# Kernel tuning notes

Hardware: AMD Instinct MI355X
Metric: run time of the kernel (lower is better)

The kernel has to match this reference:

```python
import jax, jax.numpy as jnp
import numpy as np

B, N, C_IN = 16, 1024, 768
H, KQ, VD = 8, 256, 512          # num_heads, kq_dim, v_dim per head
NH_V = H * VD                    # 4096
D_OUT = 512
SCALE = D_OUT ** -0.5            # module uses dim_out**-0.5
EPS = 1e-5


def _bn(x, gamma, beta, mean, var):
    # eval-mode BatchNorm1d over last dim
    return (x - mean) * (gamma * jax.lax.rsqrt(var + EPS)) + beta


def setup_inputs() -> dict:
    key = jax.random.key(0)
    ks = jax.random.split(key, 8)
    return {
        "x": jax.random.normal(ks[0], (B, N, C_IN), jnp.float32),
        "qkv_w": jax.random.normal(ks[1], (2 * H * KQ + NH_V, C_IN), jnp.float32) * 0.02,
        "qkv_gamma": jax.random.uniform(ks[2], (2 * H * KQ + NH_V,), jnp.float32),
        "qkv_beta": jax.random.normal(ks[3], (2 * H * KQ + NH_V,), jnp.float32) * 0.02,
        "qkv_mean": jax.random.normal(ks[4], (2 * H * KQ + NH_V,), jnp.float32) * 0.02,
        "qkv_var": jnp.ones((2 * H * KQ + NH_V,), jnp.float32),
        "pos_bias": jax.random.normal(ks[5], (H, N, N), jnp.float32),
        "proj_w": jax.random.normal(ks[6], (D_OUT, NH_V), jnp.float32) * 0.02,
        "proj_gamma": jax.random.uniform(ks[7], (D_OUT,), jnp.float32),
        "proj_beta": jnp.zeros((D_OUT,), jnp.float32),
        "proj_mean": jnp.zeros((D_OUT,), jnp.float32),
        "proj_var": jnp.ones((D_OUT,), jnp.float32),
    }


def reference(x, qkv_w, qkv_gamma, qkv_beta, qkv_mean, qkv_var,
              pos_bias, proj_w, proj_gamma, proj_beta, proj_mean, proj_var):
    b, n, _ = x.shape
    qkv = _bn(x @ qkv_w.T, qkv_gamma, qkv_beta, qkv_mean, qkv_var)  # [B,N,h]
    qkv = qkv.reshape(b, n, H, 2 * KQ + VD)
    q, k, v = jnp.split(qkv, [KQ, 2 * KQ], axis=3)                  # [B,N,H,*]
    attn = jnp.einsum('bnhd,bmhd->bhnm', q, k) * SCALE + pos_bias   # [B,H,N,N]
    attn = jax.nn.softmax(attn, axis=-1)
    out = jnp.einsum('bhnm,bmhd->bnhd', attn, v).reshape(b, n, NH_V)
    out = jnp.clip(out, -1.0, 1.0)                                  # Hardtanh
    return _bn(out @ proj_w.T, proj_gamma, proj_beta, proj_mean, proj_var)
```

## Files before the change

### kernel.cpp

```cpp
#include <hip/hip_runtime.h>

using v8bf  = __bf16 __attribute__((ext_vector_type(8)));
using v16f  = float  __attribute__((ext_vector_type(16)));

#define EPS_BN 1e-5f
#define ATT_SCALE 0.044194173824159216f

__device__ __forceinline__ unsigned short f2bf(float f){
  union { float f; unsigned int u; } c; c.f = f;
  unsigned int u = c.u + 0x7fffu + ((c.u >> 16) & 1u);
  return (unsigned short)(u >> 16);
}

__device__ __forceinline__ v8bf ld8(const unsigned short* p){
  union { uint4 u; v8bf v; } c;
  c.u = *(const uint4*)p;
  return c.v;
}

__device__ __forceinline__ void glds16(const unsigned short* g, unsigned short* l){
  __builtin_amdgcn_global_load_lds(
      (const __attribute__((address_space(1))) void*)g,
      (__attribute__((address_space(3))) void*)l, 16, 0, 0);
}

__global__ void cast_bf16_kernel(const float* __restrict__ src,
                                 unsigned short* __restrict__ dst, int n8){
  int i = blockIdx.x * 256 + threadIdx.x;
  if (i >= n8) return;
  const float4* s4 = (const float4*)src;
  float4 a = s4[2*i], b = s4[2*i+1];
  union { unsigned short s[8]; uint4 u; } r;
  r.s[0]=f2bf(a.x); r.s[1]=f2bf(a.y); r.s[2]=f2bf(a.z); r.s[3]=f2bf(a.w);
  r.s[4]=f2bf(b.x); r.s[5]=f2bf(b.y); r.s[6]=f2bf(b.z); r.s[7]=f2bf(b.w);
  ((uint4*)dst)[i] = r.u;
}

__global__ void bn_precompute(const float* __restrict__ g, const float* __restrict__ be,
                              const float* __restrict__ mn, const float* __restrict__ vr,
                              float* __restrict__ scale, float* __restrict__ shift,
                              int n, int qfold){
  int i = blockIdx.x * 256 + threadIdx.x;
  if (i >= n) return;
  float s = g[i] * rsqrtf(vr[i] + EPS_BN);
  float t = be[i] - mn[i] * s;
  if (qfold && (i & 1023) < 256){ s *= ATT_SCALE; t *= ATT_SCALE; }
  scale[i] = s; shift[i] = t;
}

template<int MODE>
__launch_bounds__(256, 2)
__global__ void gemm_nt(const unsigned short* __restrict__ A,
                        const unsigned short* __restrict__ Bm,
                        int K, long sA, long sB, long mbase,
                        const float* __restrict__ scale, const float* __restrict__ shift,
                        const float* __restrict__ sums,
                        unsigned short* __restrict__ ob16,
                        float* __restrict__ outf)
{
  __shared__ __align__(16) unsigned short As[4096];
  __shared__ __align__(16) unsigned short Bs[4096];
  const int tid = threadIdx.x;
  const int w = tid >> 6, lane = tid & 63, ln = lane & 31, lg = lane >> 5;
  const int wm = (w >> 1) * 64, wn = (w & 1) * 64;
  const long bm = (long)blockIdx.y * 128, bn = (long)blockIdx.x * 128;
  const int z = blockIdx.z;
  const unsigned short* Ab = A + (MODE == 3 ? 0L : (long)z * sA) + bm * K;
  const unsigned short* Bb = Bm + (MODE == 3 ? 0L : (long)z * sB) + bn * K;

  const int kbeg = (MODE == 3) ? z * (K >> 2) : 0;
  const int kend = (MODE == 3) ? kbeg + (K >> 2) : K;

  const int srow0 = w*32 + (lane >> 2);
  const int srow1 = srow0 + 16;
  const int slot  = lane & 3;
  const int ga0 = (slot ^ ((srow0 >> 1) & 3)) * 8;
  const int ga1 = (slot ^ ((srow1 >> 1) & 3)) * 8;
  const unsigned short* gA0 = Ab + (long)srow0 * K + ga0;
  const unsigned short* gA1 = Ab + (long)srow1 * K + ga1;
  const unsigned short* gB0 = Bb + (long)srow0 * K + ga0;
  const unsigned short* gB1 = Bb + (long)srow1 * K + ga1;
  unsigned short* lA0 = As + (w*32)*32;
  unsigned short* lA1 = As + (w*32+16)*32;
  unsigned short* lB0 = Bs + (w*32)*32;
  unsigned short* lB1 = Bs + (w*32+16)*32;

  v16f acc[2][2];
  #pragma unroll
  for (int a = 0; a < 2; a++)
    #pragma unroll
    for (int b = 0; b < 2; b++)
      #pragma unroll
      for (int i = 0; i < 16; i++) acc[a][b][i] = 0.f;

  for (int k0 = kbeg; k0 < kend; k0 += 32){
    __syncthreads();
    glds16(gA0 + k0, lA0);
    glds16(gA1 + k0, lA1);
    glds16(gB0 + k0, lB0);
    glds16(gB1 + k0, lB1);
    __syncthreads();
    #pragma unroll
    for (int kk = 0; kk < 32; kk += 16){
      v8bf af[2], bfr[2];
      #pragma unroll
      for (int t = 0; t < 2; t++){
        int Ra = wm + t*32 + ln;
        int sa = ((kk>>3) + lg) ^ ((Ra >> 1) & 3);
        af[t] = *(const v8bf*)&As[Ra*32 + sa*8];
        int Rb = wn + t*32 + ln;
        int sb = ((kk>>3) + lg) ^ ((Rb >> 1) & 3);
        bfr[t] = *(const v8bf*)&Bs[Rb*32 + sb*8];
      }
      #pragma unroll
      for (int tm = 0; tm < 2; tm++)
        #pragma unroll
        for (int tn = 0; tn < 2; tn++)
          acc[tm][tn] = __builtin_amdgcn_mfma_f32_32x32x16_bf16(af[tm], bfr[tn], acc[tm][tn], 0, 0, 0);
    }
  }

  float invs[2][16];
  if (MODE == 1){
    #pragma unroll
    for (int tm = 0; tm < 2; tm++)
      #pragma unroll
      for (int i = 0; i < 16; i++){
        long gm = bm + wm + tm*32 + (i&3) + 8*(i>>2) + 4*lg;
        invs[tm][i] = 1.0f / sums[(long)z*1024 + gm];
      }
  }

  #pragma unroll
  for (int tm = 0; tm < 2; tm++){
    #pragma unroll
    for (int tn = 0; tn < 2; tn++){
      long gn = bn + wn + tn*32 + ln;
      float sc = 0.f, sh = 0.f;
      if (MODE == 0){ sc = scale[gn]; sh = shift[gn]; }
      #pragma unroll
      for (int i = 0; i < 16; i++){
        long gm = bm + wm + tm*32 + (i&3) + 8*(i>>2) + 4*lg;
        float v = acc[tm][tn][i];
        if (MODE == 0){
          ob16[gm*8192 + gn] = f2bf(v * sc + sh);
        } else if (MODE == 1){
          v = v * invs[tm][i];
          v = fminf(1.f, fmaxf(-1.f, v));
          int b2 = z >> 3, hh = z & 7;
          ob16[((long)b2*1024 + gm)*4096 + hh*512 + gn] = f2bf(v);
        } else {
          outf[((long)z * mbase + gm)*512 + gn] = v;
        }
      }
    }
  }
}

__global__ void reduce_bn(const float* __restrict__ part,
                          const float* __restrict__ sc, const float* __restrict__ sh,
                          float* __restrict__ out, long Mtot, long mbase){
  long idx = (long)blockIdx.x * 256 + threadIdx.x;
  if (idx >= Mtot * 128) return;
  long gm = idx >> 7;
  int gn4 = (int)(idx & 127) * 4;
  long PS = Mtot * 512;
  const float* p = part + gm*512 + gn4;
  float4 p0 = *(const float4*)(p);
  float4 p1 = *(const float4*)(p + PS);
  float4 p2 = *(const float4*)(p + 2*PS);
  float4 p3 = *(const float4*)(p + 3*PS);
  float4 s4 = *(const float4*)(sc + gn4);
  float4 h4 = *(const float4*)(sh + gn4);
  float4 r;
  r.x = (p0.x+p1.x+p2.x+p3.x)*s4.x + h4.x;
  r.y = (p0.y+p1.y+p2.y+p3.y)*s4.y + h4.y;
  r.z = (p0.z+p1.z+p2.z+p3.z)*s4.z + h4.z;
  r.w = (p0.w+p1.w+p2.w+p3.w)*s4.w + h4.w;
  *(float4*)(out + (mbase + gm)*512 + gn4) = r;
}

__global__ void transpose_v(const unsigned short* __restrict__ qkv,
                            unsigned short* __restrict__ Vt){
  __shared__ __align__(16) unsigned short Ts[64*72];
  const int bh = blockIdx.z;
  const int b2 = bh >> 3, h = bh & 7;
  const int n0 = blockIdx.x * 64, d0 = blockIdx.y * 64;
  const int tid = threadIdx.x;
  const unsigned short* Vb = qkv + (long)b2*1024*8192 + h*1024 + 512;
  unsigned short* Vtb = Vt + (long)bh * 524288;
  #pragma unroll
  for (int i = 0; i < 2; i++){
    int seg = tid + i*256;
    int row = seg >> 3, co = (seg & 7) * 8;
    *(uint4*)&Ts[row*72 + co] = *(const uint4*)(Vb + (long)(n0 + row)*8192 + d0 + co);
  }
  __syncthreads();
  #pragma unroll
  for (int i = 0; i < 2; i++){
    int seg = tid + i*256;
    int drow = seg >> 3, nco = (seg & 7) * 8;
    union { unsigned short s[8]; uint4 u; } r;
    #pragma unroll
    for (int j = 0; j < 8; j++) r.s[j] = Ts[(nco + j)*72 + drow];
    *(uint4*)(Vtb + (long)(d0 + drow)*1024 + n0 + nco) = r.u;
  }
}

__launch_bounds__(256, 2)
__global__ void attn_scores(const unsigned short* __restrict__ qkv,
                            const float* __restrict__ bias,
                            unsigned short* __restrict__ E,
                            float* __restrict__ sums)
{
  __shared__ __align__(16) unsigned short Ks[2][32*256];
  const int bh = blockIdx.y, mblk = blockIdx.x;
  const int b2 = bh >> 3, h = bh & 7;
  const int tid = threadIdx.x, w = tid >> 6, lane = tid & 63, ln = lane & 31, lg = lane >> 5;
  const int m0 = mblk * 128 + w * 32;
  const unsigned short* qbase = qkv + (long)b2*1024*8192 + h*1024;
  const unsigned short* kbase = qbase + 256;
  const float* biash = bias + (long)h * 1048576;
  unsigned short* Eb = E + (long)bh * 1048576;

  v8bf qf[16];
  {
    const unsigned short* qrow = qbase + (long)(m0 + ln)*8192 + lg*8;
    #pragma unroll
    for (int kf = 0; kf < 16; kf++) qf[kf] = ld8(qrow + kf*16);
  }

  const int rr = lane >> 5, slot = lane & 31;

  float sm[16];
  #pragma unroll
  for (int i = 0; i < 16; i++) sm[i] = 0.f;

  #pragma unroll
  for (int j = 0; j < 4; j++){
    int row = w*8 + j*2 + rr;
    glds16(kbase + (long)row*8192 + (slot ^ row)*8, &Ks[0][(w*8 + j*2)*256]);
  }

  for (int t = 0; t < 32; t++){
    __syncthreads();
    const int cb = t & 1;
    if (t < 31){
      const int nb = cb ^ 1;
      #pragma unroll
      for (int j = 0; j < 4; j++){
        int row = w*8 + j*2 + rr;
        glds16(kbase + (long)((t+1)*32 + row)*8192 + (slot ^ row)*8,
               &Ks[nb][(w*8 + j*2)*256]);
      }
    }
    v16f a0, a1;
    #pragma unroll
    for (int i = 0; i < 16; i++){ a0[i] = 0.f; a1[i] = 0.f; }
    #pragma unroll
    for (int kf = 0; kf < 16; kf += 2){
      v8bf k0 = *(const v8bf*)&Ks[cb][ln*256 + ((2*kf   + lg) ^ ln)*8];
      v8bf k1 = *(const v8bf*)&Ks[cb][ln*256 + ((2*kf+2 + lg) ^ ln)*8];
      a0 = __builtin_amdgcn_mfma_f32_32x32x16_bf16(qf[kf],   k0, a0, 0, 0, 0);
      a1 = __builtin_amdgcn_mfma_f32_32x32x16_bf16(qf[kf+1], k1, a1, 0, 0, 0);
    }
    const int col = t*32 + ln;
    #pragma unroll
    for (int q = 0; q < 4; q++){
      #pragma unroll
      for (int j = 0; j < 4; j++){
        int i = q*4 + j;
        int r = 4*lg + 8*q + j;
        float e = __expf(a0[i] + a1[i] + biash[(long)(m0 + r)*1024 + col]);
        sm[i] += e;
        Eb[(long)(m0 + r)*1024 + col] = f2bf(e);
      }
    }
  }

  #pragma unroll
  for (int i = 0; i < 16; i++){
    #pragma unroll
    for (int d = 1; d < 32; d <<= 1) sm[i] += __shfl_xor(sm[i], d, 64);
  }
  if (ln == 0){
    float* sp = sums + (long)bh * 1024 + m0 + 4*lg;
    #pragma unroll
    for (int q = 0; q < 4; q++)
      #pragma unroll
      for (int j = 0; j < 4; j++)
        sp[8*q + j] = sm[q*4 + j];
  }
}

extern "C" void kernel_launch(void* const* d_in, const int* in_sizes, int n_in,
                              void* d_out, int out_size, void* d_ws, size_t ws_size,
                              hipStream_t stream)
{
  const float* x        = (const float*)d_in[0];
  const float* qkv_w    = (const float*)d_in[1];
  const float* qg       = (const float*)d_in[2];
  const float* qb       = (const float*)d_in[3];
  const float* qm       = (const float*)d_in[4];
  const float* qv       = (const float*)d_in[5];
  const float* pos_bias = (const float*)d_in[6];
  const float* pw       = (const float*)d_in[7];
  const float* pg       = (const float*)d_in[8];
  const float* pbt      = (const float*)d_in[9];
  const float* pmn      = (const float*)d_in[10];
  const float* pvr      = (const float*)d_in[11];
  float* out = (float*)d_out;

  const unsigned long FIXED = 16846848UL;
  const unsigned long PERG  = 43548672UL;
  long G = 1;
  if      (ws_size >= FIXED + PERG*16) G = 16;
  else if (ws_size >= FIXED + PERG*8)  G = 8;
  else if (ws_size >= FIXED + PERG*4)  G = 4;
  else if (ws_size >= FIXED + PERG*2)  G = 2;
  else if (ws_size >= FIXED + PERG)    G = 1;
  else return;

  char* ws = (char*)d_ws;
  unsigned short* wqb = (unsigned short*)(ws + 0L);
  unsigned short* wpb = (unsigned short*)(ws + 12582912L);
  float* sc_qkv       = (float*)(ws + 16777216L);
  float* sh_qkv       = (float*)(ws + 16809984L);
  float* sc_p         = (float*)(ws + 16842752L);
  float* sh_p         = (float*)(ws + 16844800L);
  const long gb = 16846848L;
  unsigned short* xbg   = (unsigned short*)(ws + gb);
  unsigned short* qkvg  = (unsigned short*)(ws + gb + G*1572864L);
  unsigned short* Vtg   = (unsigned short*)(ws + gb + G*18350080L);
  unsigned short* Eg    = (unsigned short*)(ws + gb + G*26738688L);
  float* sumsg          = (float*)(ws + gb + G*43515904L);
  unsigned short* outcg = qkvg;
  float* partials       = (float*)Eg;

  cast_bf16_kernel<<<dim3(3072), 256, 0, stream>>>(qkv_w, wqb, 786432);
  cast_bf16_kernel<<<dim3(1024), 256, 0, stream>>>(pw,    wpb, 262144);
  bn_precompute<<<dim3(32), 256, 0, stream>>>(qg, qb, qm, qv, sc_qkv, sh_qkv, 8192, 1);
  bn_precompute<<<dim3(2),  256, 0, stream>>>(pg, pbt, pmn, pvr, sc_p, sh_p, 512, 0);

  const int nG = (int)(16 / G);
  for (int g = 0; g < nG; g++){
    const float* xg = x + (long)g * G * 786432L;
    long mbase = (long)g * G * 1024L;

    cast_bf16_kernel<<<dim3((unsigned)(G*384)), 256, 0, stream>>>(xg, xbg, (int)(G*98304));

    gemm_nt<0><<<dim3(64, (unsigned)(8*G), 1), 256, 0, stream>>>(
        xbg, wqb, 768, 0L, 0L, 0L, sc_qkv, sh_qkv, nullptr, qkvg, nullptr);

    transpose_v<<<dim3(16, 8, (unsigned)(8*G)), 256, 0, stream>>>(qkvg, Vtg);

    attn_scores<<<dim3(8, (unsigned)(8*G)), 256, 0, stream>>>(qkvg, pos_bias, Eg, sumsg);

    gemm_nt<1><<<dim3(4, 8, (unsigned)(8*G)), 256, 0, stream>>>(
        Eg, Vtg, 1024, 1048576L, 524288L, 0L, nullptr, nullptr, sumsg, outcg, nullptr);

    gemm_nt<3><<<dim3(4, (unsigned)(8*G), 4), 256, 0, stream>>>(
        outcg, wpb, 4096, 0L, 0L, (long)(G*1024), nullptr, nullptr, nullptr,
        nullptr, partials);

    reduce_bn<<<dim3((unsigned)(G*512)), 256, 0, stream>>>(
        partials, sc_p, sh_p, out, (long)(G*1024), mbase);
  }
}
```

Measured before the change: 1.127 ms.

## Double GEMM K-tile to 64 and halve attn_scores block size

The bf16 GEMM now stages a 64-wide K slice per iteration instead of 32, using an 8-slot XOR swizzle over 64-element LDS rows. This halves the number of barrier pairs per K loop at the cost of twice the LDS per block. Separately, attn_scores now runs 128-thread blocks covering 64 query rows, with twice as many blocks. Each wave loads more K rows so the block can still fill the shared K tile. Smaller blocks may improve occupancy and load balance, but each K tile is now reused by fewer query rows.

```diff
diff --git a/kernel.cpp b/kernel.cpp
--- a/kernel.cpp
+++ b/kernel.cpp
@@ -58,8 +58,8 @@
                         unsigned short* __restrict__ ob16,
                         float* __restrict__ outf)
 {
-  __shared__ __align__(16) unsigned short As[4096];
-  __shared__ __align__(16) unsigned short Bs[4096];
+  __shared__ __align__(16) unsigned short As[8192];
+  __shared__ __align__(16) unsigned short Bs[8192];
   const int tid = threadIdx.x;
   const int w = tid >> 6, lane = tid & 63, ln = lane & 31, lg = lane >> 5;
   const int wm = (w >> 1) * 64, wn = (w & 1) * 64;
@@ -71,19 +71,19 @@
   const int kbeg = (MODE == 3) ? z * (K >> 2) : 0;
   const int kend = (MODE == 3) ? kbeg + (K >> 2) : K;
 
-  const int srow0 = w*32 + (lane >> 2);
-  const int srow1 = srow0 + 16;
-  const int slot  = lane & 3;
-  const int ga0 = (slot ^ ((srow0 >> 1) & 3)) * 8;
-  const int ga1 = (slot ^ ((srow1 >> 1) & 3)) * 8;
-  const unsigned short* gA0 = Ab + (long)srow0 * K + ga0;
-  const unsigned short* gA1 = Ab + (long)srow1 * K + ga1;
-  const unsigned short* gB0 = Bb + (long)srow0 * K + ga0;
-  const unsigned short* gB1 = Bb + (long)srow1 * K + ga1;
-  unsigned short* lA0 = As + (w*32)*32;
-  unsigned short* lA1 = As + (w*32+16)*32;
-  unsigned short* lB0 = Bs + (w*32)*32;
-  unsigned short* lB1 = Bs + (w*32+16)*32;
+  const int rsub = lane >> 3;
+  const int gsl  = lane & 7;
+  const unsigned short* gA[4]; const unsigned short* gB[4];
+  unsigned short *lA[4], *lB[4];
+  #pragma unroll
+  for (int i = 0; i < 4; i++){
+    int r = w*32 + i*8 + rsub;
+    int go = (gsl ^ (r & 7)) * 8;
+    gA[i] = Ab + (long)r * K + go;
+    gB[i] = Bb + (long)r * K + go;
+    lA[i] = As + (w*32 + i*8) * 64;
+    lB[i] = Bs + (w*32 + i*8) * 64;
+  }
 
   v16f acc[2][2];
   #pragma unroll
@@ -93,24 +93,23 @@
       #pragma unroll
       for (int i = 0; i < 16; i++) acc[a][b][i] = 0.f;
 
-  for (int k0 = kbeg; k0 < kend; k0 += 32){
+  for (int k0 = kbeg; k0 < kend; k0 += 64){
     __syncthreads();
-    glds16(gA0 + k0, lA0);
-    glds16(gA1 + k0, lA1);
-    glds16(gB0 + k0, lB0);
-    glds16(gB1 + k0, lB1);
+    #pragma unroll
+    for (int i = 0; i < 4; i++){
+      glds16(gA[i] + k0, lA[i]);
+      glds16(gB[i] + k0, lB[i]);
+    }
     __syncthreads();
     #pragma unroll
-    for (int kk = 0; kk < 32; kk += 16){
+    for (int kk = 0; kk < 4; kk++){
       v8bf af[2], bfr[2];
       #pragma unroll
       for (int t = 0; t < 2; t++){
         int Ra = wm + t*32 + ln;
-        int sa = ((kk>>3) + lg) ^ ((Ra >> 1) & 3);
-        af[t] = *(const v8bf*)&As[Ra*32 + sa*8];
+        af[t] = *(const v8bf*)&As[Ra*64 + ((kk*2 + lg) ^ (Ra & 7))*8];
         int Rb = wn + t*32 + ln;
-        int sb = ((kk>>3) + lg) ^ ((Rb >> 1) & 3);
-        bfr[t] = *(const v8bf*)&Bs[Rb*32 + sb*8];
+        bfr[t] = *(const v8bf*)&Bs[Rb*64 + ((kk*2 + lg) ^ (Rb & 7))*8];
       }
       #pragma unroll
       for (int tm = 0; tm < 2; tm++)
@@ -207,7 +206,7 @@
   }
 }
 
-__launch_bounds__(256, 2)
+__launch_bounds__(128, 2)
 __global__ void attn_scores(const unsigned short* __restrict__ qkv,
                             const float* __restrict__ bias,
                             unsigned short* __restrict__ E,
@@ -217,7 +216,7 @@
   const int bh = blockIdx.y, mblk = blockIdx.x;
   const int b2 = bh >> 3, h = bh & 7;
   const int tid = threadIdx.x, w = tid >> 6, lane = tid & 63, ln = lane & 31, lg = lane >> 5;
-  const int m0 = mblk * 128 + w * 32;
+  const int m0 = mblk * 64 + w * 32;
   const unsigned short* qbase = qkv + (long)b2*1024*8192 + h*1024;
   const unsigned short* kbase = qbase + 256;
   const float* biash = bias + (long)h * 1048576;
@@ -237,9 +236,9 @@
   for (int i = 0; i < 16; i++) sm[i] = 0.f;
 
   #pragma unroll
-  for (int j = 0; j < 4; j++){
-    int row = w*8 + j*2 + rr;
-    glds16(kbase + (long)row*8192 + (slot ^ row)*8, &Ks[0][(w*8 + j*2)*256]);
+  for (int i = 0; i < 8; i++){
+    int row = w*16 + i*2 + rr;
+    glds16(kbase + (long)row*8192 + (slot ^ row)*8, &Ks[0][(w*16 + i*2)*256]);
   }
 
   for (int t = 0; t < 32; t++){
@@ -248,10 +247,10 @@
     if (t < 31){
       const int nb = cb ^ 1;
       #pragma unroll
-      for (int j = 0; j < 4; j++){
-        int row = w*8 + j*2 + rr;
+      for (int i = 0; i < 8; i++){
+        int row = w*16 + i*2 + rr;
         glds16(kbase + (long)((t+1)*32 + row)*8192 + (slot ^ row)*8,
-               &Ks[nb][(w*8 + j*2)*256]);
+               &Ks[nb][(w*16 + i*2)*256]);
       }
     }
     v16f a0, a1;
@@ -354,7 +353,7 @@
 
     transpose_v<<<dim3(16, 8, (unsigned)(8*G)), 256, 0, stream>>>(qkvg, Vtg);
 
-    attn_scores<<<dim3(8, (unsigned)(8*G)), 256, 0, stream>>>(qkvg, pos_bias, Eg, sumsg);
+    attn_scores<<<dim3(16, (unsigned)(8*G)), 128, 0, stream>>>(qkvg, pos_bias, Eg, sumsg);
 
     gemm_nt<1><<<dim3(4, 8, (unsigned)(8*G)), 256, 0, stream>>>(
         Eg, Vtg, 1024, 1048576L, 524288L, 0L, nullptr, nullptr, sumsg, outcg, nullptr);
```

Result: faster. 1.063 ms (-5.7%).
